# Kernel optimization log

Hardware: AMD Instinct MI355X
Metric: run time of the kernel (lower is better)

Reference implementation:

```python
import jax, jax.numpy as jnp
import numpy as np

EPS = 1e-5

def _face_normals(v, vi):
    # v: [B,V,3], vi: [F,3] -> [B,F,3]
    pts = v[:, vi]                                  # [B,F,3,3]
    n = jnp.cross(pts[:, :, 1] - pts[:, :, 0], pts[:, :, 2] - pts[:, :, 0])
    norm = jnp.linalg.norm(n, axis=-1, keepdims=True)
    return n / jnp.where(norm < EPS, 1.0, norm)

def _vert_normals(v, vi):
    fn = _face_normals(v, vi)                       # [B,F,3]
    fn_rep = jnp.repeat(fn, 3, axis=1)              # [B,3F,3] (one copy per face vertex)
    vn = jnp.zeros_like(v).at[:, vi.reshape(-1)].add(fn_rep)
    norm = jnp.linalg.norm(vn, axis=-1, keepdims=True)
    return vn / jnp.where(norm < EPS, 1.0, norm)

def _values_to_uv(values, index_image, bary_image):
    # values: [B,V,C]; index_image/bary_image: [U,U,3] -> [B,C,U,U]
    mask = jnp.all(index_image != -1, axis=-1)      # [U,U]
    idx = jnp.clip(index_image, 0, values.shape[1] - 1)
    vals = values[:, idx]                           # [B,U,U,3,C]
    uv = jnp.einsum('buvkc,uvk->bcuv', vals, bary_image.astype(values.dtype))
    return uv * mask[None, None].astype(values.dtype)

def _grid_sample_bilinear(img, gx, gy):
    # img: [B,C,H,W]; gx,gy: [N] in [-1,1]; align_corners=False, zero padding
    B, C, H, W = img.shape
    ix = ((gx + 1.0) * W - 1.0) * 0.5
    iy = ((gy + 1.0) * H - 1.0) * 0.5
    x0 = jnp.floor(ix); y0 = jnp.floor(iy)
    x1 = x0 + 1.0;      y1 = y0 + 1.0
    wx1 = ix - x0; wx0 = 1.0 - wx1
    wy1 = iy - y0; wy0 = 1.0 - wy1
    def gather(xi, yi):
        valid = (xi >= 0) & (xi < W) & (yi >= 0) & (yi < H)
        xc = jnp.clip(xi, 0, W - 1).astype(jnp.int32)
        yc = jnp.clip(yi, 0, H - 1).astype(jnp.int32)
        return img[:, :, yc, xc] * valid.astype(img.dtype)  # [B,C,N]
    return (gather(x0, y0) * (wx0 * wy0) + gather(x1, y0) * (wx1 * wy0)
          + gather(x0, y1) * (wx0 * wy1) + gather(x1, y1) * (wx1 * wy1))

def _sample_uv(values_uv, uv_coords, v2uv):
    g = uv_coords * 2.0 - 1.0                       # [T,2]
    vals = _grid_sample_bilinear(values_uv, g[:, 0], g[:, 1])  # [B,C,T]
    vals = jnp.transpose(vals, (0, 2, 1))           # [B,T,C]
    return vals[:, v2uv].mean(axis=2)               # [B,V,C]

def setup_inputs() -> dict:
    key = jax.random.key(0)
    ks = jax.random.split(key, 6)
    B, V, Fc, U, T, K = 8, 100000, 200000, 1024, 110000, 2
    verts = jax.random.normal(ks[0], (B, V, 3), jnp.float32)
    vi = jax.random.randint(ks[1], (Fc, 3), 0, V, dtype=jnp.int32)
    index_image = jax.random.randint(ks[2], (U, U, 3), 0, V, dtype=jnp.int32)
    bary_image = jax.random.uniform(ks[3], (U, U, 3), jnp.float32)
    vt = jax.random.uniform(ks[4], (T, 2), jnp.float32)
    v2uv = jax.random.randint(ks[5], (V, K), 0, T, dtype=jnp.int32)
    return {"verts": verts, "bary_image": bary_image, "vt": vt,
            "vi": vi, "index_image": index_image, "v2uv": v2uv}

def reference(verts, bary_image, vt, vi, index_image, v2uv):
    vn = _vert_normals(verts, vi)                   # [B,V,3]
    uv = _values_to_uv(vn, index_image, bary_image) # [B,3,U,U]
    return _sample_uv(uv, vt, v2uv)                 # [B,V,3]
```

## Files before the change

kernel.cpp:

```cpp
#include <hip/hip_runtime.h>

#define EPS 1e-5f

constexpr int B = 8;
constexpr int V = 100000;
constexpr int F = 200000;
constexpr int U = 1024;
constexpr int T = 110000;
constexpr int ELLCAP = 32;

__global__ void transpose_verts(const float* __restrict__ verts,
                                float* __restrict__ vertsT) {
    int v = blockIdx.x * blockDim.x + threadIdx.x;
    if (v >= V) return;
    float buf[24];
#pragma unroll
    for (int b = 0; b < 8; ++b) {
        const float* p = verts + (size_t)b * V * 3 + (size_t)v * 3;
        buf[b * 3 + 0] = p[0];
        buf[b * 3 + 1] = p[1];
        buf[b * 3 + 2] = p[2];
    }
    float4* dst = (float4*)(vertsT + (size_t)v * 24);
    const float4* src = (const float4*)buf;
#pragma unroll
    for (int i = 0; i < 6; ++i) dst[i] = src[i];
}

__global__ void ell_fill(const int* __restrict__ vi,
                         int* __restrict__ cnt,
                         int* __restrict__ ell) {
    int e = blockIdx.x * blockDim.x + threadIdx.x;
    if (e >= 3 * F) return;
    int v = vi[e];
    int pos = atomicAdd(&cnt[v], 1);
    if (pos < ELLCAP) ell[v * ELLCAP + pos] = e / 3;
}

__global__ void gather_vn(const float* __restrict__ vertsT,
                          const int* __restrict__ vi,
                          const int* __restrict__ cnt,
                          const int* __restrict__ ell,
                          float4* __restrict__ vn) {
    int id = blockIdx.x * blockDim.x + threadIdx.x;
    if (id >= V * 8) return;
    int v = id >> 3;
    int b = id & 7;

    int deg = min(cnt[v], ELLCAP);
    const int* row = ell + (size_t)v * ELLCAP;

    float ax = 0.0f, ay = 0.0f, az = 0.0f;
    for (int j = 0; j < deg; ++j) {
        int f = row[j];
        int i0 = vi[f * 3 + 0];
        int i1 = vi[f * 3 + 1];
        int i2 = vi[f * 3 + 2];

        const float* p0 = vertsT + (size_t)i0 * 24 + b * 3;
        const float* p1 = vertsT + (size_t)i1 * 24 + b * 3;
        const float* p2 = vertsT + (size_t)i2 * 24 + b * 3;

        float ox = p0[0], oy = p0[1], oz = p0[2];
        float e1x = p1[0] - ox, e1y = p1[1] - oy, e1z = p1[2] - oz;
        float e2x = p2[0] - ox, e2y = p2[1] - oy, e2z = p2[2] - oz;

        float nx = e1y * e2z - e1z * e2y;
        float ny = e1z * e2x - e1x * e2z;
        float nz = e1x * e2y - e1y * e2x;

        float norm = sqrtf(nx * nx + ny * ny + nz * nz);
        float inv = (norm < EPS) ? 1.0f : (1.0f / norm);
        ax += nx * inv; ay += ny * inv; az += nz * inv;
    }

    float n = sqrtf(ax * ax + ay * ay + az * az);
    float inv = (n < EPS) ? 1.0f : (1.0f / n);
    vn[id] = make_float4(ax * inv, ay * inv, az * inv, 0.0f);
}

__global__ void sample_points(const float4* __restrict__ vn,
                              const int* __restrict__ index_image,
                              const float* __restrict__ bary_image,
                              const float* __restrict__ vt,
                              float4* __restrict__ vals) {
    int id = blockIdx.x * blockDim.x + threadIdx.x;
    if (id >= T * 8) return;
    int t = id >> 3;
    int b = id & 7;

    float gx = vt[t * 2 + 0];
    float gy = vt[t * 2 + 1];
    float ix = gx * (float)U - 0.5f;
    float iy = gy * (float)U - 0.5f;

    float x0f = floorf(ix);
    float y0f = floorf(iy);
    int x0 = (int)x0f;
    int y0 = (int)y0f;
    float wx1 = ix - x0f, wx0 = 1.0f - wx1;
    float wy1 = iy - y0f, wy0 = 1.0f - wy1;

    float ax = 0.0f, ay = 0.0f, az = 0.0f;

#pragma unroll
    for (int cy = 0; cy < 2; ++cy) {
        int y = y0 + cy;
        if (y < 0 || y >= U) continue;
        float wy = cy ? wy1 : wy0;
#pragma unroll
        for (int cx = 0; cx < 2; ++cx) {
            int x = x0 + cx;
            if (x < 0 || x >= U) continue;
            float w = wy * (cx ? wx1 : wx0);

            int pix = y * U + x;
            int i0 = index_image[pix * 3 + 0];
            int i1 = index_image[pix * 3 + 1];
            int i2 = index_image[pix * 3 + 2];
            float m = (i0 != -1 && i1 != -1 && i2 != -1) ? 1.0f : 0.0f;
            i0 = min(max(i0, 0), V - 1);
            i1 = min(max(i1, 0), V - 1);
            i2 = min(max(i2, 0), V - 1);

            float b0 = bary_image[pix * 3 + 0];
            float b1 = bary_image[pix * 3 + 1];
            float b2 = bary_image[pix * 3 + 2];

            float4 q0 = vn[(size_t)i0 * 8 + b];
            float4 q1 = vn[(size_t)i1 * 8 + b];
            float4 q2 = vn[(size_t)i2 * 8 + b];

            float wm = w * m;
            float wb0 = wm * b0, wb1 = wm * b1, wb2 = wm * b2;
            ax += wb0 * q0.x + wb1 * q1.x + wb2 * q2.x;
            ay += wb0 * q0.y + wb1 * q1.y + wb2 * q2.y;
            az += wb0 * q0.z + wb1 * q1.z + wb2 * q2.z;
        }
    }

    vals[id] = make_float4(ax, ay, az, 0.0f);
}

__global__ void gather_out(const float4* __restrict__ vals,
                           const int* __restrict__ v2uv,
                           float* __restrict__ out) {
    int id = blockIdx.x * blockDim.x + threadIdx.x;
    if (id >= V * 8) return;
    int v = id >> 3;
    int b = id & 7;

    int t0 = v2uv[v * 2 + 0];
    int t1 = v2uv[v * 2 + 1];
    float4 x = vals[(size_t)t0 * 8 + b];
    float4 y = vals[(size_t)t1 * 8 + b];

    float* o = out + (size_t)b * V * 3 + (size_t)v * 3;
    o[0] = 0.5f * (x.x + y.x);
    o[1] = 0.5f * (x.y + y.y);
    o[2] = 0.5f * (x.z + y.z);
}

extern "C" void kernel_launch(void* const* d_in, const int* in_sizes, int n_in,
                              void* d_out, int out_size, void* d_ws, size_t ws_size,
                              hipStream_t stream) {
    const float* verts   = (const float*)d_in[0];
    const float* bary    = (const float*)d_in[1];
    const float* vt      = (const float*)d_in[2];
    const int*   vi      = (const int*)d_in[3];
    const int*   idx_img = (const int*)d_in[4];
    const int*   v2uv    = (const int*)d_in[5];
    float* out = (float*)d_out;

    float* vertsT = (float*)d_ws;
    float* vals   = (float*)d_ws;
    float* vn     = vals + (size_t)T * 8 * 4;
    int*   cnt    = (int*)(vn + (size_t)V * 8 * 4);
    int*   ell    = cnt + V;

    hipMemsetAsync(cnt, 0, (size_t)V * sizeof(int), stream);

    const int BLK = 256;
    transpose_verts<<<(V + BLK - 1) / BLK, BLK, 0, stream>>>(verts, vertsT);
    ell_fill<<<(3 * F + BLK - 1) / BLK, BLK, 0, stream>>>(vi, cnt, ell);
    gather_vn<<<(V * 8 + BLK - 1) / BLK, BLK, 0, stream>>>(
        vertsT, vi, cnt, ell, (float4*)vn);
    sample_points<<<(T * 8 + BLK - 1) / BLK, BLK, 0, stream>>>(
        (const float4*)vn, idx_img, bary, vt, (float4*)vals);
    gather_out<<<(V * 8 + BLK - 1) / BLK, BLK, 0, stream>>>(
        (const float4*)vals, v2uv, out);
}
```

Measured before the change: 212.7 us.

## Precompute face normals once and gather them per vertex; fuse preprocessing kernels

Adds a face_normals kernel that computes each normalized face normal once per batch into a float4 buffer. gather_vn then sums these per incident face instead of recomputing the cross product from three vertex gathers per adjacency. The vertex transpose now pads rows to float4 and is merged with the ELL fill into a single launch. This trades redundant scattered vertex loads and math for one extra intermediate buffer write and read.

```diff
diff --git a/kernel.cpp b/kernel.cpp
--- a/kernel.cpp
+++ b/kernel.cpp
@@ -8,37 +8,65 @@
 constexpr int U = 1024;
 constexpr int T = 110000;
 constexpr int ELLCAP = 32;
-
-__global__ void transpose_verts(const float* __restrict__ verts,
-                                float* __restrict__ vertsT) {
-    int v = blockIdx.x * blockDim.x + threadIdx.x;
-    if (v >= V) return;
-    float buf[24];
-#pragma unroll
-    for (int b = 0; b < 8; ++b) {
-        const float* p = verts + (size_t)b * V * 3 + (size_t)v * 3;
-        buf[b * 3 + 0] = p[0];
-        buf[b * 3 + 1] = p[1];
-        buf[b * 3 + 2] = p[2];
+constexpr int TRB = (V + 255) / 256;
+constexpr int ELB = (3 * F + 255) / 256;
+
+__global__ void pre_kernel(const float* __restrict__ verts,
+                           float4* __restrict__ vertsT,
+                           const int* __restrict__ vi,
+                           int* __restrict__ cnt,
+                           int* __restrict__ ell) {
+    int blk = blockIdx.x;
+    if (blk < TRB) {
+        int v = blk * 256 + threadIdx.x;
+        if (v >= V) return;
+        float4 row[8];
+#pragma unroll
+        for (int b = 0; b < 8; ++b) {
+            const float* p = verts + (size_t)b * V * 3 + (size_t)v * 3;
+            row[b] = make_float4(p[0], p[1], p[2], 0.0f);
+        }
+        float4* dst = vertsT + (size_t)v * 8;
+#pragma unroll
+        for (int b = 0; b < 8; ++b) dst[b] = row[b];
+    } else {
+        int e = (blk - TRB) * 256 + threadIdx.x;
+        if (e >= 3 * F) return;
+        int v = vi[e];
+        int pos = atomicAdd(&cnt[v], 1);
+        if (pos < ELLCAP) ell[v * ELLCAP + pos] = e / 3;
     }
-    float4* dst = (float4*)(vertsT + (size_t)v * 24);
-    const float4* src = (const float4*)buf;
-#pragma unroll
-    for (int i = 0; i < 6; ++i) dst[i] = src[i];
-}
-
-__global__ void ell_fill(const int* __restrict__ vi,
-                         int* __restrict__ cnt,
-                         int* __restrict__ ell) {
-    int e = blockIdx.x * blockDim.x + threadIdx.x;
-    if (e >= 3 * F) return;
-    int v = vi[e];
-    int pos = atomicAdd(&cnt[v], 1);
-    if (pos < ELLCAP) ell[v * ELLCAP + pos] = e / 3;
-}
-
-__global__ void gather_vn(const float* __restrict__ vertsT,
-                          const int* __restrict__ vi,
+}
+
+__global__ void face_normals(const float4* __restrict__ vertsT,
+                             const int* __restrict__ vi,
+                             float4* __restrict__ fn) {
+    int id = blockIdx.x * blockDim.x + threadIdx.x;
+    if (id >= F * 8) return;
+    int f = id >> 3;
+    int b = id & 7;
+
+    int i0 = vi[f * 3 + 0];
+    int i1 = vi[f * 3 + 1];
+    int i2 = vi[f * 3 + 2];
+
+    float4 p0 = vertsT[(size_t)i0 * 8 + b];
+    float4 p1 = vertsT[(size_t)i1 * 8 + b];
+    float4 p2 = vertsT[(size_t)i2 * 8 + b];
+
+    float e1x = p1.x - p0.x, e1y = p1.y - p0.y, e1z = p1.z - p0.z;
+    float e2x = p2.x - p0.x, e2y = p2.y - p0.y, e2z = p2.z - p0.z;
+
+    float nx = e1y * e2z - e1z * e2y;
+    float ny = e1z * e2x - e1x * e2z;
+    float nz = e1x * e2y - e1y * e2x;
+
+    float norm = sqrtf(nx * nx + ny * ny + nz * nz);
+    float inv = (norm < EPS) ? 1.0f : (1.0f / norm);
+    fn[id] = make_float4(nx * inv, ny * inv, nz * inv, 0.0f);
+}
+
+__global__ void gather_vn(const float4* __restrict__ fn,
                           const int* __restrict__ cnt,
                           const int* __restrict__ ell,
                           float4* __restrict__ vn) {
@@ -53,25 +81,8 @@
     float ax = 0.0f, ay = 0.0f, az = 0.0f;
     for (int j = 0; j < deg; ++j) {
         int f = row[j];
-        int i0 = vi[f * 3 + 0];
-        int i1 = vi[f * 3 + 1];
-        int i2 = vi[f * 3 + 2];
-
-        const float* p0 = vertsT + (size_t)i0 * 24 + b * 3;
-        const float* p1 = vertsT + (size_t)i1 * 24 + b * 3;
-        const float* p2 = vertsT + (size_t)i2 * 24 + b * 3;
-
-        float ox = p0[0], oy = p0[1], oz = p0[2];
-        float e1x = p1[0] - ox, e1y = p1[1] - oy, e1z = p1[2] - oz;
-        float e2x = p2[0] - ox, e2y = p2[1] - oy, e2z = p2[2] - oz;
-
-        float nx = e1y * e2z - e1z * e2y;
-        float ny = e1z * e2x - e1x * e2z;
-        float nz = e1x * e2y - e1y * e2x;
-
-        float norm = sqrtf(nx * nx + ny * ny + nz * nz);
-        float inv = (norm < EPS) ? 1.0f : (1.0f / norm);
-        ax += nx * inv; ay += ny * inv; az += nz * inv;
+        float4 n = fn[(size_t)f * 8 + b];
+        ax += n.x; ay += n.y; az += n.z;
     }
 
     float n = sqrtf(ax * ax + ay * ay + az * az);
@@ -172,21 +183,20 @@
     const int*   v2uv    = (const int*)d_in[5];
     float* out = (float*)d_out;
 
-    float* vertsT = (float*)d_ws;
-    float* vals   = (float*)d_ws;
-    float* vn     = vals + (size_t)T * 8 * 4;
-    int*   cnt    = (int*)(vn + (size_t)V * 8 * 4);
-    int*   ell    = cnt + V;
+    float4* vertsT = (float4*)d_ws;
+    float4* vn     = vertsT;
+    float4* fn     = vertsT + (size_t)V * 8;
+    float4* vals   = fn;
+    int*    cnt    = (int*)(fn + (size_t)F * 8);
+    int*    ell    = cnt + V;
 
     hipMemsetAsync(cnt, 0, (size_t)V * sizeof(int), stream);
 
     const int BLK = 256;
-    transpose_verts<<<(V + BLK - 1) / BLK, BLK, 0, stream>>>(verts, vertsT);
-    ell_fill<<<(3 * F + BLK - 1) / BLK, BLK, 0, stream>>>(vi, cnt, ell);
-    gather_vn<<<(V * 8 + BLK - 1) / BLK, BLK, 0, stream>>>(
-        vertsT, vi, cnt, ell, (float4*)vn);
+    pre_kernel<<<TRB + ELB, BLK, 0, stream>>>(verts, vertsT, vi, cnt, ell);
+    face_normals<<<(F * 8 + BLK - 1) / BLK, BLK, 0, stream>>>(vertsT, vi, fn);
+    gather_vn<<<(V * 8 + BLK - 1) / BLK, BLK, 0, stream>>>(fn, cnt, ell, vn);
     sample_points<<<(T * 8 + BLK - 1) / BLK, BLK, 0, stream>>>(
-        (const float4*)vn, idx_img, bary, vt, (float4*)vals);
-    gather_out<<<(V * 8 + BLK - 1) / BLK, BLK, 0, stream>>>(
-        (const float4*)vals, v2uv, out);
-}
+        vn, idx_img, bary, vt, vals);
+    gather_out<<<(V * 8 + BLK - 1) / BLK, BLK, 0, stream>>>(vals, v2uv, out);
+}
```

Measured after the change: 207.8 us. 2.3% less time.
